# Performance work log

Hardware: AMD Instinct MI355X
Metric: run time of the kernel (lower is better)

The kernel has to match this reference:

```python
import jax, jax.numpy as jnp
import numpy as np

B = 1
T, H, W = 8, 20, 20
N = T * H * W  # 3200
DIM = 3072
NH = 24
HD = DIM // NH  # 128
D_T, D_H, D_W = 32, 48, 48  # 3D RoPE split of head_dim
EPS = 1e-6


def _axis_freqs(d, n):
    # [n, d//2] angles for one axis
    inv = 1.0 / (10000.0 ** (jnp.arange(0, d, 2, dtype=jnp.float32) / d))
    return jnp.arange(n, dtype=jnp.float32)[:, None] * inv[None, :]


def rope3d_cos_sin(t, h, w):
    ft = jnp.broadcast_to(_axis_freqs(D_T, t)[:, None, None, :], (t, h, w, D_T // 2))
    fh = jnp.broadcast_to(_axis_freqs(D_H, h)[None, :, None, :], (t, h, w, D_H // 2))
    fw = jnp.broadcast_to(_axis_freqs(D_W, w)[None, None, :, :], (t, h, w, D_W // 2))
    f = jnp.concatenate([ft, fh, fw], axis=-1).reshape(t * h * w, HD // 2)
    return jnp.cos(f), jnp.sin(f)


def apply_rope(x, cos, sin):
    # x: [B, N, NH, HD]; interleaved pairs rotation
    xf = x.astype(jnp.float32).reshape(*x.shape[:-1], HD // 2, 2)
    x1, x2 = xf[..., 0], xf[..., 1]
    c = cos[None, :, None, :]
    s = sin[None, :, None, :]
    r1 = x1 * c - x2 * s
    r2 = x1 * s + x2 * c
    return jnp.stack([r1, r2], axis=-1).reshape(x.shape).astype(x.dtype)


def rmsnorm(x, w):
    xf = x.astype(jnp.float32)
    n = xf * jax.lax.rsqrt(jnp.mean(xf * xf, axis=-1, keepdims=True) + EPS)
    return (n * w).astype(x.dtype)


def setup_inputs() -> dict:
    key = jax.random.key(0)
    ks = jax.random.split(key, 6)
    scale = 0.02
    return {
        "x": jax.random.normal(ks[0], (B, N, DIM), jnp.float32),
        "Wq": jax.random.normal(ks[1], (DIM, DIM), jnp.float32) * scale,
        "bq": jnp.zeros((DIM,), jnp.float32),
        "Wk": jax.random.normal(ks[2], (DIM, DIM), jnp.float32) * scale,
        "bk": jnp.zeros((DIM,), jnp.float32),
        "Wv": jax.random.normal(ks[3], (DIM, DIM), jnp.float32) * scale,
        "bv": jnp.zeros((DIM,), jnp.float32),
        "Wo": jax.random.normal(ks[4], (DIM, DIM), jnp.float32) * scale,
        "bo": jnp.zeros((DIM,), jnp.float32),
        "q_norm_w": jnp.ones((HD,), jnp.float32),
        "k_norm_w": jnp.ones((HD,), jnp.float32),
        "num_cond_latents": 2,
    }


def reference(x, Wq, bq, Wk, bk, Wv, bv, Wo, bo, q_norm_w, k_norm_w, num_cond_latents):
    # QKV projections -> [B, N, NH, HD]
    q = (x @ Wq + bq).reshape(B, N, NH, HD)
    k = (x @ Wk + bk).reshape(B, N, NH, HD)
    v = (x @ Wv + bv).reshape(B, N, NH, HD)
    # per-head RMSNorm on q, k
    q = rmsnorm(q, q_norm_w)
    k = rmsnorm(k, k_norm_w)
    # 3D RoPE over (T, H, W) grid
    cos, sin = rope3d_cos_sin(T, H, W)
    q = apply_rope(q, cos, sin)
    k = apply_rope(k, cos, sin)
    # I2V split: cond tokens attend only to themselves; noise tokens attend to all
    nct = num_cond_latents * (N // T)  # static python int
    out_cond = jax.nn.dot_product_attention(q[:, :nct], k[:, :nct], v[:, :nct])
    out_noise = jax.nn.dot_product_attention(q[:, nct:], k, v)
    out = jnp.concatenate([out_cond, out_noise], axis=1).reshape(B, N, DIM)
    return out @ Wo + bo
```

## Files before the change

### kernel.cpp

```cpp
#include <hip/hip_runtime.h>
#include <stdint.h>

typedef _Float16 f16;
typedef _Float16 f16x2 __attribute__((ext_vector_type(2)));
typedef _Float16 f16x4 __attribute__((ext_vector_type(4)));
typedef _Float16 f16x8 __attribute__((ext_vector_type(8)));
typedef float f32x4 __attribute__((ext_vector_type(4)));
typedef float f32x16 __attribute__((ext_vector_type(16)));

#define DIM   3072
#define NTOK  3200
#define NHEAD 24
#define SCALE 0.08838834764831845f
#define LOG2E 1.4426950408889634f

__device__ __forceinline__ void async16(const void* g, void* l) {
  __builtin_amdgcn_global_load_lds(
      (const __attribute__((address_space(1))) uint32_t*)g,
      (__attribute__((address_space(3))) uint32_t*)l, 16, 0, 0);
}

__device__ __forceinline__ uint32_t pkrtz(float a, float b) {
  auto p = __builtin_amdgcn_cvt_pkrtz(a, b);
  return __builtin_bit_cast(uint32_t, p);
}

__device__ __forceinline__ float fexp2(float x) {
  float r;
  asm("v_exp_f32 %0, %1" : "=v"(r) : "v"(x));
  return r;
}

__device__ __forceinline__ f32x4 mfma16(f16x8 a, f16x8 b, f32x4 c) {
  return __builtin_amdgcn_mfma_f32_16x16x32_f16(a, b, c, 0, 0, 0);
}

__device__ __forceinline__ int xcd_remap(int orig, int nwg) {
  int q = nwg >> 3, r = nwg & 7;
  int xcd = orig & 7;
  int base = xcd < r ? xcd * (q + 1) : r * (q + 1) + (xcd - r) * q;
  return base + (orig >> 3);
}


__global__ __launch_bounds__(256) void cvt_f32_f16(const float* __restrict__ in,
                                                   f16* __restrict__ out) {
  size_t i = ((size_t)blockIdx.x * 256 + threadIdx.x) * 4;
  float4 v = *(const float4*)(in + i);
  f16x4 o = {(f16)v.x, (f16)v.y, (f16)v.z, (f16)v.w};
  *(f16x4*)(out + i) = o;
}

__global__ __launch_bounds__(256) void transpose4(
    const float* __restrict__ W0, const float* __restrict__ W1,
    const float* __restrict__ W2, const float* __restrict__ W3,
    f16* __restrict__ T0, f16* __restrict__ T1,
    f16* __restrict__ T2, f16* __restrict__ T3) {
  const float* W; f16* T;
  switch (blockIdx.z) {
    case 0: W = W0; T = T0; break;
    case 1: W = W1; T = T1; break;
    case 2: W = W2; T = T2; break;
    default: W = W3; T = T3; break;
  }
  __shared__ float t[32][33];
  int tx = threadIdx.x & 31, ty = threadIdx.x >> 5;
  size_t bx = (size_t)blockIdx.x * 32, by = (size_t)blockIdx.y * 32;
#pragma unroll
  for (int r = 0; r < 4; ++r)
    t[ty + r * 8][tx] = W[(by + ty + r * 8) * DIM + bx + tx];
  __syncthreads();
#pragma unroll
  for (int r = 0; r < 4; ++r)
    T[(bx + ty + r * 8) * DIM + by + tx] = (f16)t[tx][ty + r * 8];
}

__global__ __launch_bounds__(256) void rope_tables(float* __restrict__ cosT,
                                                   float* __restrict__ sinT) {
  int tid = blockIdx.x * 256 + threadIdx.x;
  int p = tid >> 6, j = tid & 63;
  int t = p / 400, rem = p % 400;
  int hh = rem / 20, ww = rem % 20;
  float val, e;
  if (j < 16)      { val = (float)t;  e = (float)(2 * j)        * (1.f / 32.f); }
  else if (j < 40) { val = (float)hh; e = (float)(2 * (j - 16)) * (1.f / 48.f); }
  else             { val = (float)ww; e = (float)(2 * (j - 40)) * (1.f / 48.f); }
  float f = val * expf(-e * 9.210340371976184f);
  cosT[tid] = cosf(f);
  sinT[tid] = sinf(f);
}


__device__ __forceinline__ void stage_half(const f16* __restrict__ base, int row0,
                                           int rowmax, int k0, char* ldsdst, int tid) {
#pragma unroll
  for (int s = 0; s < 2; ++s) {
    int idx = s * 512 + tid;
    int r = idx >> 3, pc = idx & 7;
    int cc = pc ^ (r & 7);
    int grow = row0 + r;
    grow = grow < rowmax ? grow : rowmax - 1;
    async16(base + (size_t)grow * DIM + k0 + cc * 8, ldsdst + idx * 16);
  }
}

__device__ __forceinline__ void gemm256_body(
    const f16* __restrict__ A, const f16* __restrict__ Bm,
    const float* __restrict__ bias, void* __restrict__ C,
    int m0, int n0, int Mrows, int mode, char* smem) {

  const int tid = threadIdx.x;
  const int lane = tid & 63, w = tid >> 6;
  const int wm = w >> 2, wn = w & 3;
  const int l15 = lane & 15, l4 = lane >> 4;

  f32x4 acc[8][4];
#pragma unroll
  for (int m = 0; m < 8; ++m)
#pragma unroll
    for (int n = 0; n < 4; ++n) acc[m][n] = (f32x4){0.f, 0.f, 0.f, 0.f};

  const int NT = DIM / 64;

  stage_half(A,  m0,       Mrows,   0,  smem + 0,     tid);
  stage_half(Bm, n0,       1 << 30, 0,  smem + 32768, tid);
  stage_half(A,  m0 + 128, Mrows,   0,  smem + 16384, tid);
  stage_half(Bm, n0 + 128, 1 << 30, 0,  smem + 49152, tid);
  stage_half(A,  m0,       Mrows,   64, smem + 65536, tid);
  asm volatile("s_waitcnt vmcnt(2)" ::: "memory");
  __builtin_amdgcn_s_barrier();

  const int arow0 = wm * 128 + l15;
  const int brow0 = wn * 64 + l15;

  for (int t = 0; t < NT; ++t) {
    char* bufc = smem + (t & 1) * 65536;
    char* bufn = smem + ((t + 1) & 1) * 65536;
    const f16* Ald = (const f16*)bufc;
    const f16* Bld = (const f16*)(bufc + 32768);
    int k1 = (t + 1) * 64; k1 = k1 <= DIM - 64 ? k1 : DIM - 64;
    int k2 = (t + 2) * 64; k2 = k2 <= DIM - 64 ? k2 : DIM - 64;

    f16x8 af[8], b0, b1;

#pragma unroll
    for (int m = 0; m < 8; ++m) {
      int r = arow0 + m * 16, pc = l4 ^ (r & 7);
      af[m] = *(const f16x8*)(Ald + r * 64 + pc * 8);
    }
    { int r = brow0,      pc = l4 ^ (r & 7); b0 = *(const f16x8*)(Bld + r * 64 + pc * 8);
      r = brow0 + 16;     pc = l4 ^ (r & 7); b1 = *(const f16x8*)(Bld + r * 64 + pc * 8); }
    stage_half(Bm, n0, 1 << 30, k1, bufn + 32768, tid);
    __builtin_amdgcn_s_barrier();
    asm volatile("s_waitcnt lgkmcnt(0)" ::: "memory");
    __builtin_amdgcn_sched_barrier(0);
    __builtin_amdgcn_s_setprio(1);
#pragma unroll
    for (int m = 0; m < 8; ++m) {
      acc[m][0] = mfma16(af[m], b0, acc[m][0]);
      acc[m][1] = mfma16(af[m], b1, acc[m][1]);
    }
    __builtin_amdgcn_s_setprio(0);
    __builtin_amdgcn_s_barrier();

    { int r = brow0 + 32, pc = l4 ^ (r & 7); b0 = *(const f16x8*)(Bld + r * 64 + pc * 8);
      r = brow0 + 48;     pc = l4 ^ (r & 7); b1 = *(const f16x8*)(Bld + r * 64 + pc * 8); }
    stage_half(A, m0 + 128, Mrows, k1, bufn + 16384, tid);
    __builtin_amdgcn_s_barrier();
    asm volatile("s_waitcnt lgkmcnt(0)" ::: "memory");
    __builtin_amdgcn_sched_barrier(0);
    __builtin_amdgcn_s_setprio(1);
#pragma unroll
    for (int m = 0; m < 8; ++m) {
      acc[m][2] = mfma16(af[m], b0, acc[m][2]);
      acc[m][3] = mfma16(af[m], b1, acc[m][3]);
    }
    __builtin_amdgcn_s_setprio(0);
    __builtin_amdgcn_s_barrier();

#pragma unroll
    for (int m = 0; m < 8; ++m) {
      int r = arow0 + m * 16, pc = (4 + l4) ^ (r & 7);
      af[m] = *(const f16x8*)(Ald + r * 64 + pc * 8);
    }
    { int r = brow0,      pc = (4 + l4) ^ (r & 7); b0 = *(const f16x8*)(Bld + r * 64 + pc * 8);
      r = brow0 + 16;     pc = (4 + l4) ^ (r & 7); b1 = *(const f16x8*)(Bld + r * 64 + pc * 8); }
    stage_half(Bm, n0 + 128, 1 << 30, k1, bufn + 49152, tid);
    __builtin_amdgcn_s_barrier();
    asm volatile("s_waitcnt lgkmcnt(0)" ::: "memory");
    __builtin_amdgcn_sched_barrier(0);
    __builtin_amdgcn_s_setprio(1);
#pragma unroll
    for (int m = 0; m < 8; ++m) {
      acc[m][0] = mfma16(af[m], b0, acc[m][0]);
      acc[m][1] = mfma16(af[m], b1, acc[m][1]);
    }
    __builtin_amdgcn_s_setprio(0);
    __builtin_amdgcn_s_barrier();

    { int r = brow0 + 32, pc = (4 + l4) ^ (r & 7); b0 = *(const f16x8*)(Bld + r * 64 + pc * 8);
      r = brow0 + 48;     pc = (4 + l4) ^ (r & 7); b1 = *(const f16x8*)(Bld + r * 64 + pc * 8); }
    stage_half(A, m0, Mrows, k2, bufc + 0, tid);
    __builtin_amdgcn_s_barrier();
    asm volatile("s_waitcnt lgkmcnt(0)" ::: "memory");
    __builtin_amdgcn_sched_barrier(0);
    __builtin_amdgcn_s_setprio(1);
#pragma unroll
    for (int m = 0; m < 8; ++m) {
      acc[m][2] = mfma16(af[m], b0, acc[m][2]);
      acc[m][3] = mfma16(af[m], b1, acc[m][3]);
    }
    __builtin_amdgcn_s_setprio(0);
    asm volatile("s_waitcnt vmcnt(2)" ::: "memory");
    __builtin_amdgcn_s_barrier();
  }

#pragma unroll
  for (int n = 0; n < 4; ++n) {
    int col = n0 + wn * 64 + n * 16 + l15;
    float bb = bias[col];
#pragma unroll
    for (int m = 0; m < 8; ++m) {
      int rbase = m0 + wm * 128 + m * 16 + l4 * 4;
      if (rbase < Mrows) {
        if (mode == 2) {
          f16x4 ov;
#pragma unroll
          for (int r = 0; r < 4; ++r) ov[r] = (f16)(acc[m][n][r] + bb);
          *(f16x4*)((f16*)C + (size_t)col * NTOK + rbase) = ov;
        } else if (mode == 1) {
#pragma unroll
          for (int r = 0; r < 4; ++r)
            ((float*)C)[(size_t)(rbase + r) * DIM + col] = acc[m][n][r] + bb;
        } else {
#pragma unroll
          for (int r = 0; r < 4; ++r)
            ((f16*)C)[(size_t)(rbase + r) * DIM + col] = (f16)(acc[m][n][r] + bb);
        }
      }
    }
  }
}

__global__ __launch_bounds__(512, 2) void gemm256_qkv(
    const f16* __restrict__ A,
    const f16* __restrict__ B0, const f16* __restrict__ B1, const f16* __restrict__ B2,
    const float* __restrict__ b0, const float* __restrict__ b1, const float* __restrict__ b2,
    f16* __restrict__ C0, f16* __restrict__ C1, f16* __restrict__ C2) {
  __shared__ char smem[131072];
  int wgid = xcd_remap(blockIdx.y * 13 + blockIdx.x, 13 * 36);
  int mt = wgid % 13, yy = wgid / 13;
  int sel = yy / 12, yn = yy % 12;
  const f16* B = sel == 0 ? B0 : (sel == 1 ? B1 : B2);
  const float* bias = sel == 0 ? b0 : (sel == 1 ? b1 : b2);
  f16* C = sel == 0 ? C0 : (sel == 1 ? C1 : C2);
  gemm256_body(A, B, bias, C, mt * 256, yn * 256, NTOK, sel == 2 ? 2 : 0, smem);
}

__global__ __launch_bounds__(512, 2) void gemm256_out(
    const f16* __restrict__ A, const f16* __restrict__ B,
    const float* __restrict__ bias, float* __restrict__ C) {
  __shared__ char smem[131072];
  int wgid = xcd_remap(blockIdx.y * 13 + blockIdx.x, 13 * 12);
  int mt = wgid % 13, ny = wgid / 13;
  gemm256_body(A, B, bias, C, mt * 256, ny * 256, NTOK, 1, smem);
}

__global__ __launch_bounds__(256) void rmsnorm_rope2(
    f16* __restrict__ qbuf, f16* __restrict__ kbuf,
    const float* __restrict__ qw, const float* __restrict__ kw,
    const float* __restrict__ cosT, const float* __restrict__ sinT) {
  f16* qk = blockIdx.y ? kbuf : qbuf;
  const float* w = blockIdx.y ? kw : qw;
  const float osc = blockIdx.y ? 1.0f : SCALE * LOG2E;
  int lane = threadIdx.x & 63, rb = threadIdx.x >> 6;
  int row = blockIdx.x * 4 + rb;
  int p = row / NHEAD;
  f16* ptr = qk + (size_t)row * 128 + lane * 2;
  f16x2 hv = *(const f16x2*)ptr;
  float x1 = (float)hv[0], x2 = (float)hv[1];
  float ss = x1 * x1 + x2 * x2;
#pragma unroll
  for (int o = 32; o > 0; o >>= 1) ss += __shfl_xor(ss, o);
  float r = rsqrtf(ss * (1.f / 128.f) + 1e-6f);
  float n1 = x1 * r * w[lane * 2], n2 = x2 * r * w[lane * 2 + 1];
  float c = cosT[p * 64 + lane], s = sinT[p * 64 + lane];
  f16x2 ov = {(f16)((n1 * c - n2 * s) * osc), (f16)((n1 * s + n2 * c) * osc)};
  *(f16x2*)ptr = ov;
}

__global__ __launch_bounds__(320) void attn7(
    const f16* __restrict__ q, const f16* __restrict__ k, const f16* __restrict__ vt,
    f16* __restrict__ out, f16* __restrict__ Op, float2* __restrict__ ml) {
  __shared__ char smem[65536];
  f16* Ks = (f16*)smem;
  f16* Vs = (f16*)(smem + 32768);

  int L = blockIdx.x;
  int xcd = L & 7, j = L >> 3;
  int head = xcd * 3 + j / 35;
  int u = j % 35;
  int q0, kv_lo, kv_hi, s = 0;
  bool direct;
  if (u < 5) { q0 = u * 160; kv_lo = 0; kv_hi = 800; direct = true; }
  else {
    int v = u - 5;
    int qn = v >> 1; s = v & 1;
    q0 = 800 + qn * 160; kv_lo = s * 1600; kv_hi = kv_lo + 1600; direct = false;
  }

  const int tid = threadIdx.x, lane = tid & 63, w = tid >> 6;
  const int l31 = lane & 31, hi = lane >> 5;
  const int qg = q0 + w * 32 + l31;
  const int sw_base = l31 & 15;

  f16x8 qr[8];
#pragma unroll
  for (int ks = 0; ks < 8; ++ks)
    qr[ks] = *(const f16x8*)(q + (size_t)qg * DIM + head * 128 + ks * 16 + hi * 8);

  const f16x8 ones = {(f16)1, (f16)1, (f16)1, (f16)1, (f16)1, (f16)1, (f16)1, (f16)1};

  f32x16 o[4], lsum;
#pragma unroll
  for (int mb = 0; mb < 4; ++mb)
#pragma unroll
    for (int r = 0; r < 16; ++r) o[mb][r] = 0.f;
#pragma unroll
  for (int r = 0; r < 16; ++r) lsum[r] = 0.f;
  float m_run = -1e30f;

  for (int t0 = kv_lo; t0 < kv_hi; t0 += 128) {
    __syncthreads();
#pragma unroll
    for (int r = 0; r < 13; ++r) {
      int idx = r * 320 + tid;
      if (idx < 4096) {
        int row = (idx >> 4) & 127;
        int sw = (idx & 15) ^ (row & 15);
        const f16* src;
        if (idx < 2048) src = k + (size_t)(t0 + row) * DIM + head * 128 + sw * 8;
        else            src = vt + ((size_t)head * 128 + row) * NTOK + t0 + sw * 8;
        async16(src, smem + idx * 16);
      }
    }
    __syncthreads();

    const int nvb = min(4, (kv_hi - t0) >> 5);

    f32x16 s4[4];
#pragma unroll
    for (int b = 0; b < 4; ++b)
#pragma unroll
      for (int r = 0; r < 16; ++r) s4[b][r] = 0.f;
    __builtin_amdgcn_s_setprio(1);
#pragma unroll
    for (int ks = 0; ks < 8; ++ks) {
#pragma unroll
      for (int b = 0; b < 4; ++b) {
        if (b < nvb) {
          const f16x8 kf = *(const f16x8*)(Ks + ((b * 32 + l31) << 7) +
                                           (((ks * 2 + hi) ^ sw_base) << 3));
          s4[b] = __builtin_amdgcn_mfma_f32_32x32x16_f16(kf, qr[ks], s4[b], 0, 0, 0);
        }
      }
    }
    __builtin_amdgcn_s_setprio(0);

    float tmax = -1e30f;
#pragma unroll
    for (int b = 0; b < 4; ++b)
      if (b < nvb)
#pragma unroll
        for (int r = 0; r < 16; r += 2)
          tmax = fmaxf(tmax, fmaxf(s4[b][r], s4[b][r + 1]));
    tmax = fmaxf(tmax, __shfl_xor(tmax, 32));
    if (!__all(tmax <= m_run + 11.54f)) {
      float mn = fmaxf(m_run, tmax);
      float alpha = fexp2(m_run - mn);
#pragma unroll
      for (int mb = 0; mb < 4; ++mb)
#pragma unroll
        for (int r = 0; r < 16; ++r) o[mb][r] *= alpha;
#pragma unroll
      for (int r = 0; r < 16; ++r) lsum[r] *= alpha;
      m_run = mn;
    }

#pragma unroll
    for (int r = 0; r < 16; ++r) s4[0][r] = fexp2(s4[0][r] - m_run);

    const int nks = nvb * 2;
    __builtin_amdgcn_s_setprio(1);
#pragma unroll
    for (int ks = 0; ks < 8; ++ks) {
      if (ks < nks) {
        const int b = ks >> 1, s8 = (ks & 1) * 8;
        if ((ks & 1) && (b + 1) < nvb) {
#pragma unroll
          for (int r = 0; r < 16; ++r)
            s4[b + 1][r] = fexp2(s4[b + 1][r] - m_run);
        }
        uint32_t a0 = pkrtz(s4[b][s8 + 0], s4[b][s8 + 1]);
        uint32_t b0 = pkrtz(s4[b][s8 + 4], s4[b][s8 + 5]);
        asm("v_permlane32_swap_b32 %0, %1" : "+v"(a0), "+v"(b0));
        uint32_t a1 = pkrtz(s4[b][s8 + 2], s4[b][s8 + 3]);
        uint32_t b1 = pkrtz(s4[b][s8 + 6], s4[b][s8 + 7]);
        asm("v_permlane32_swap_b32 %0, %1" : "+v"(a1), "+v"(b1));
        union { uint32_t u[4]; f16x8 v; } pf;
        pf.u[0] = a0; pf.u[1] = a1; pf.u[2] = b0; pf.u[3] = b1;
#pragma unroll
        for (int mb = 0; mb < 4; ++mb) {
          const f16x8 vf = *(const f16x8*)(Vs + ((mb * 32 + l31) << 7) +
                                           (((ks * 2 + hi) ^ sw_base) << 3));
          o[mb] = __builtin_amdgcn_mfma_f32_32x32x16_f16(vf, pf.v, o[mb], 0, 0, 0);
        }
        lsum = __builtin_amdgcn_mfma_f32_32x32x16_f16(ones, pf.v, lsum, 0, 0, 0);
      }
    }
    __builtin_amdgcn_s_setprio(0);
  }

  float inv = 1.f / lsum[0];
  f16* obase = direct
      ? out + (size_t)qg * DIM + head * 128
      : Op + ((size_t)(s * NHEAD + head) * 2400 + (qg - 800)) * 128;
#pragma unroll
  for (int mb = 0; mb < 4; ++mb)
#pragma unroll
    for (int jq = 0; jq < 4; ++jq) {
      f16x4 ov;
#pragma unroll
      for (int e = 0; e < 4; ++e) ov[e] = (f16)(o[mb][jq * 4 + e] * inv);
      *(f16x4*)(obase + mb * 32 + jq * 8 + hi * 4) = ov;
    }
  if (!direct && hi == 0)
    ml[(size_t)(s * NHEAD + head) * 2400 + (qg - 800)] = make_float2(m_run, lsum[0]);
}

__global__ __launch_bounds__(256) void attn_merge(
    const f16* __restrict__ Op, const float2* __restrict__ ml,
    f16* __restrict__ out) {
  int row = blockIdx.x * 4 + (threadIdx.x >> 6);
  int lane = threadIdx.x & 63;
  int head = row / 2400, qn = row % 2400;
  float2 ml1 = ml[row];
  float2 ml2 = ml[24 * 2400 + row];
  float m = fmaxf(ml1.x, ml2.x);
  float w1 = ml1.y * fexp2(ml1.x - m);
  float w2 = ml2.y * fexp2(ml2.x - m);
  float inv = 1.f / (w1 + w2);
  w1 *= inv; w2 *= inv;
  f16x2 o1 = *(const f16x2*)(Op + (size_t)row * 128 + lane * 2);
  f16x2 o2 = *(const f16x2*)(Op + (size_t)(24 * 2400 + row) * 128 + lane * 2);
  f16x2 ov = {(f16)((float)o1[0] * w1 + (float)o2[0] * w2),
              (f16)((float)o1[1] * w1 + (float)o2[1] * w2)};
  *(f16x2*)(out + (size_t)(800 + qn) * DIM + head * 128 + lane * 2) = ov;
}


extern "C" void kernel_launch(void* const* d_in, const int* in_sizes, int n_in,
                              void* d_out, int out_size, void* d_ws, size_t ws_size,
                              hipStream_t stream) {
  const float* x   = (const float*)d_in[0];
  const float* Wq  = (const float*)d_in[1];
  const float* bq  = (const float*)d_in[2];
  const float* Wk  = (const float*)d_in[3];
  const float* bk  = (const float*)d_in[4];
  const float* Wv  = (const float*)d_in[5];
  const float* bv  = (const float*)d_in[6];
  const float* Wo  = (const float*)d_in[7];
  const float* bo  = (const float*)d_in[8];
  const float* qnw = (const float*)d_in[9];
  const float* knw = (const float*)d_in[10];

  char* ws = (char*)d_ws;
  f16*   xb   = (f16*)(ws);
  f16*   WqT  = (f16*)(ws + 19660800);
  f16*   WkT  = (f16*)(ws + 38535168);
  f16*   WvT  = (f16*)(ws + 57409536);
  f16*   WoT  = (f16*)(ws + 76283904);
  f16*   qb   = (f16*)(ws + 95158272);
  f16*   kb   = (f16*)(ws + 114819072);
  f16*   vtb  = (f16*)(ws + 134479872);
  f16*   ab   = (f16*)(ws + 154140672);
  float* cosT = (float*)(ws + 173801472);
  float* sinT = (float*)(ws + 174620672);
  f16*    Op  = (f16*)(ws);
  float2* ml  = (float2*)(ws + 29491200);

  cvt_f32_f16<<<9600, 256, 0, stream>>>(x, xb);
  transpose4<<<dim3(96, 96, 4), 256, 0, stream>>>(Wq, Wk, Wv, Wo, WqT, WkT, WvT, WoT);
  rope_tables<<<800, 256, 0, stream>>>(cosT, sinT);

  gemm256_qkv<<<dim3(13, 36), 512, 0, stream>>>(xb, WqT, WkT, WvT, bq, bk, bv, qb, kb, vtb);

  rmsnorm_rope2<<<dim3(19200, 2), 256, 0, stream>>>(qb, kb, qnw, knw, cosT, sinT);

  attn7<<<840, 320, 0, stream>>>(qb, kb, vtb, ab, Op, ml);
  attn_merge<<<14400, 256, 0, stream>>>(Op, ml, ab);

  gemm256_out<<<dim3(13, 12), 512, 0, stream>>>(ab, WoT, bo, (float*)d_out);
}
```

Measured before the change: 536.7 us.

## Prefetch next KV tile into registers during attention compute; reorder block schedule

```diff
diff --git a/kernel.cpp b/kernel.cpp
--- a/kernel.cpp
+++ b/kernel.cpp
@@ -289,7 +289,7 @@
   *(f16x2*)ptr = ov;
 }
 
-__global__ __launch_bounds__(320) void attn7(
+__global__ __launch_bounds__(320) void attn9(
     const f16* __restrict__ q, const f16* __restrict__ k, const f16* __restrict__ vt,
     f16* __restrict__ out, f16* __restrict__ Op, float2* __restrict__ ml) {
   __shared__ char smem[65536];
@@ -302,11 +302,11 @@
   int u = j % 35;
   int q0, kv_lo, kv_hi, s = 0;
   bool direct;
-  if (u < 5) { q0 = u * 160; kv_lo = 0; kv_hi = 800; direct = true; }
-  else {
-    int v = u - 5;
-    int qn = v >> 1; s = v & 1;
+  if (u < 30) {
+    int qn = u >> 1; s = u & 1;
     q0 = 800 + qn * 160; kv_lo = s * 1600; kv_hi = kv_lo + 1600; direct = false;
+  } else {
+    q0 = (u - 30) * 160; kv_lo = 0; kv_hi = 800; direct = true;
   }
 
   const int tid = threadIdx.x, lane = tid & 63, w = tid >> 6;
@@ -330,23 +330,23 @@
   for (int r = 0; r < 16; ++r) lsum[r] = 0.f;
   float m_run = -1e30f;
 
+#pragma unroll
+  for (int r = 0; r < 13; ++r) {
+    int idx = r * 320 + tid;
+    if (idx < 4096) {
+      int row = (idx >> 4) & 127;
+      int sw = (idx & 15) ^ (row & 15);
+      const f16* src;
+      if (idx < 2048) src = k + (size_t)(kv_lo + row) * DIM + head * 128 + sw * 8;
+      else            src = vt + ((size_t)head * 128 + row) * NTOK + kv_lo + sw * 8;
+      async16(src, smem + idx * 16);
+    }
+  }
+  __syncthreads();
+
   for (int t0 = kv_lo; t0 < kv_hi; t0 += 128) {
-    __syncthreads();
-#pragma unroll
-    for (int r = 0; r < 13; ++r) {
-      int idx = r * 320 + tid;
-      if (idx < 4096) {
-        int row = (idx >> 4) & 127;
-        int sw = (idx & 15) ^ (row & 15);
-        const f16* src;
-        if (idx < 2048) src = k + (size_t)(t0 + row) * DIM + head * 128 + sw * 8;
-        else            src = vt + ((size_t)head * 128 + row) * NTOK + t0 + sw * 8;
-        async16(src, smem + idx * 16);
-      }
-    }
-    __syncthreads();
-
     const int nvb = min(4, (kv_hi - t0) >> 5);
+    const bool pf = (t0 + 128) < kv_hi;
 
     f32x16 s4[4];
 #pragma unroll
@@ -366,6 +366,23 @@
       }
     }
     __builtin_amdgcn_s_setprio(0);
+
+    uint4 stg[13];
+    if (pf) {
+      const int tn = t0 + 128;
+#pragma unroll
+      for (int r = 0; r < 13; ++r) {
+        int idx = r * 320 + tid;
+        if (idx < 4096) {
+          int row = (idx >> 4) & 127;
+          int sw = (idx & 15) ^ (row & 15);
+          const f16* src;
+          if (idx < 2048) src = k + (size_t)(tn + row) * DIM + head * 128 + sw * 8;
+          else            src = vt + ((size_t)head * 128 + row) * NTOK + tn + sw * 8;
+          stg[r] = *(const uint4*)src;
+        }
+      }
+    }
 
     float tmax = -1e30f;
 #pragma unroll
@@ -407,18 +424,28 @@
         uint32_t a1 = pkrtz(s4[b][s8 + 2], s4[b][s8 + 3]);
         uint32_t b1 = pkrtz(s4[b][s8 + 6], s4[b][s8 + 7]);
         asm("v_permlane32_swap_b32 %0, %1" : "+v"(a1), "+v"(b1));
-        union { uint32_t u[4]; f16x8 v; } pf;
-        pf.u[0] = a0; pf.u[1] = a1; pf.u[2] = b0; pf.u[3] = b1;
+        union { uint32_t u[4]; f16x8 v; } pf2;
+        pf2.u[0] = a0; pf2.u[1] = a1; pf2.u[2] = b0; pf2.u[3] = b1;
 #pragma unroll
         for (int mb = 0; mb < 4; ++mb) {
           const f16x8 vf = *(const f16x8*)(Vs + ((mb * 32 + l31) << 7) +
                                            (((ks * 2 + hi) ^ sw_base) << 3));
-          o[mb] = __builtin_amdgcn_mfma_f32_32x32x16_f16(vf, pf.v, o[mb], 0, 0, 0);
+          o[mb] = __builtin_amdgcn_mfma_f32_32x32x16_f16(vf, pf2.v, o[mb], 0, 0, 0);
         }
-        lsum = __builtin_amdgcn_mfma_f32_32x32x16_f16(ones, pf.v, lsum, 0, 0, 0);
+        lsum = __builtin_amdgcn_mfma_f32_32x32x16_f16(ones, pf2.v, lsum, 0, 0, 0);
       }
     }
     __builtin_amdgcn_s_setprio(0);
+
+    __syncthreads();
+    if (pf) {
+#pragma unroll
+      for (int r = 0; r < 13; ++r) {
+        int idx = r * 320 + tid;
+        if (idx < 4096) *(uint4*)(smem + idx * 16) = stg[r];
+      }
+    }
+    __syncthreads();
   }
 
   float inv = 1.f / lsum[0];
@@ -497,7 +524,7 @@
 
   rmsnorm_rope2<<<dim3(19200, 2), 256, 0, stream>>>(qb, kb, qnw, knw, cosT, sinT);
 
-  attn7<<<840, 320, 0, stream>>>(qb, kb, vtb, ab, Op, ml);
+  attn9<<<840, 320, 0, stream>>>(qb, kb, vtb, ab, Op, ml);
   attn_merge<<<14400, 256, 0, stream>>>(Op, ml, ab);
 
   gemm256_out<<<dim3(13, 12), 512, 0, stream>>>(ab, WoT, bo, (float*)d_out);
```

Result: slower. 798.7 us (+48.8%).
